# Kernel tuning notes

Hardware: AMD Instinct MI355X
Metric: run time of the kernel (lower is better)

Reference implementation:

```python
import jax, jax.numpy as jnp
import numpy as np

RES = 1024
NUM_ROOMS = 8
N_AGENTS = 5_000_000


def setup_inputs() -> dict:
    key = jax.random.key(0)
    k1, k2, k3 = jax.random.split(key, 3)
    agent_positions = jax.random.uniform(k1, (N_AGENTS, 2), dtype=jnp.float32)
    room_params = jax.random.uniform(k2, (NUM_ROOMS, 4), dtype=jnp.float32)
    # torch init: params[:, 2:] = params[:, 2:] * 0.1 + 0.05  (room sigmas)
    room_params = room_params.at[:, 2:].set(room_params[:, 2:] * 0.1 + 0.05)
    wall_density = jax.random.uniform(k3, (RES, RES), dtype=jnp.float32)
    return {
        "agent_positions": agent_positions,
        "room_params": room_params,
        "wall_density": wall_density,
    }


def reference(agent_positions, room_params, wall_density):
    res = wall_density.shape[0]
    lin = jnp.linspace(0.0, 1.0, res, dtype=wall_density.dtype)
    x_grid, y_grid = jnp.meshgrid(lin, lin, indexing="ij")  # [res,res]

    # Per-room Gaussian density maps, vectorized over rooms -> [R,res,res]
    cx = room_params[:, 0, None, None]
    cy = room_params[:, 1, None, None]
    sx = room_params[:, 2, None, None]
    sy = room_params[:, 3, None, None]
    spatial_layout = jnp.exp(
        -((x_grid - cx) ** 2 / (2.0 * sx**2) + (y_grid - cy) ** 2 / (2.0 * sy**2))
    )

    # Agent flow histogram via single fused scatter-add
    ix = jnp.clip((agent_positions[:, 0] * res).astype(jnp.int32), 0, res - 1)
    iy = jnp.clip((agent_positions[:, 1] * res).astype(jnp.int32), 0, res - 1)
    flow_field = jnp.zeros((res, res), dtype=wall_density.dtype).at[ix, iy].add(1.0)
    flow_field = flow_field / (flow_field.max() + 1e-6)

    dynamic_layout = spatial_layout * (1.0 - wall_density[None, :, :])
    return (dynamic_layout, flow_field)
```

## Files before the change

kernel.cpp:

```cpp
#include <hip/hip_runtime.h>

#define RES 1024
#define NROOMS 8
#define NBUCKETS 256
#define BINS_PER_BUCKET (4 * RES)
#define CAP 32768
#define SWPB 8
#define F4PT 8
#define AGB 8192

__global__ __launch_bounds__(512) void scatter_kernel(
    const float4* __restrict__ pos, int n4, int nagents,
    unsigned short* __restrict__ buf, unsigned int* __restrict__ cursor)
{
    __shared__ unsigned int   cnt[SWPB][NBUCKETS];
    __shared__ unsigned int   sbase[SWPB][NBUCKETS];
    __shared__ unsigned int   pstart[NBUCKETS];
    __shared__ unsigned int   ptotal[NBUCKETS];
    __shared__ unsigned int   gbase[NBUCKETS];
    __shared__ unsigned int   wsum[4];
    __shared__ unsigned short staged[AGB];

    int tid  = threadIdx.x;
    int wv   = tid >> 6;
    int lane = tid & 63;

    #pragma unroll
    for (int i = 0; i < (SWPB * NBUCKETS) / 512; ++i)
        ((unsigned int*)cnt)[tid + 512 * i] = 0u;
    __syncthreads();

    unsigned int   code[2 * F4PT];
    unsigned short rank[2 * F4PT];
    int base4 = blockIdx.x * (AGB / 2);
    #pragma unroll
    for (int k = 0; k < F4PT; ++k) {
        int i4 = base4 + (k << 9) + tid;
        if (i4 < n4) {
            float4 p = pos[i4];
            int ix0 = min(max((int)(p.x * 1024.0f), 0), 1023);
            int iy0 = min(max((int)(p.y * 1024.0f), 0), 1023);
            int ix1 = min(max((int)(p.z * 1024.0f), 0), 1023);
            int iy1 = min(max((int)(p.w * 1024.0f), 0), 1023);
            unsigned int b0 = (unsigned int)(ix0 >> 2);
            unsigned int b1 = (unsigned int)(ix1 >> 2);
            code[2 * k]     = (b0 << 16) | (unsigned int)(((ix0 & 3) << 10) | iy0);
            code[2 * k + 1] = (b1 << 16) | (unsigned int)(((ix1 & 3) << 10) | iy1);
            rank[2 * k]     = (unsigned short)atomicAdd(&cnt[wv][b0], 1u);
            rank[2 * k + 1] = (unsigned short)atomicAdd(&cnt[wv][b1], 1u);
        } else {
            code[2 * k] = 0xFFFFFFFFu;
            code[2 * k + 1] = 0xFFFFFFFFu;
        }
    }
    __syncthreads();

    unsigned int run = 0;
    if (tid < NBUCKETS) {
        #pragma unroll
        for (int w = 0; w < SWPB; ++w) {
            unsigned int c = cnt[w][tid];
            sbase[w][tid] = run;
            run += c;
        }
        ptotal[tid] = run;
        gbase[tid]  = run ? atomicAdd(&cursor[tid], run) : 0u;
        unsigned int t = run;
        #pragma unroll
        for (int off = 1; off < 64; off <<= 1) {
            unsigned int v = (unsigned int)__shfl_up((int)t, off, 64);
            if (lane >= off) t += v;
        }
        if (lane == 63) wsum[wv] = t;
        pstart[tid] = t - run;
    }
    __syncthreads();
    if (tid < NBUCKETS) {
        unsigned int off = 0;
        #pragma unroll
        for (int w = 0; w < 3; ++w) if (w < wv) off += wsum[w];
        unsigned int ps = pstart[tid] + off;
        pstart[tid] = ps;
        #pragma unroll
        for (int w = 0; w < SWPB; ++w) sbase[w][tid] += ps;
    }
    __syncthreads();

    #pragma unroll
    for (int k = 0; k < 2 * F4PT; ++k) {
        unsigned int cd = code[k];
        if (cd != 0xFFFFFFFFu) {
            unsigned int b = cd >> 16;
            staged[sbase[wv][b] + rank[k]] = (unsigned short)(cd & 0xFFFFu);
        }
    }
    __syncthreads();

    #pragma unroll 4
    for (int bb = 0; bb < 32; ++bb) {
        int b = (wv << 5) + bb;
        unsigned int n  = ptotal[b];
        unsigned int ps = pstart[b];
        unsigned int gb = gbase[b];
        for (unsigned int e = lane; e < n; e += 64) {
            unsigned int p = gb + e;
            if (p < CAP) buf[b * CAP + p] = staged[ps + e];
        }
    }

    if (blockIdx.x == 0 && tid == 0 && (nagents & 1)) {
        const float* t = (const float*)pos;
        float px = t[2 * (nagents - 1)];
        float py = t[2 * (nagents - 1) + 1];
        int ix = min(max((int)(px * 1024.0f), 0), 1023);
        int iy = min(max((int)(py * 1024.0f), 0), 1023);
        unsigned int b = (unsigned int)(ix >> 2);
        unsigned int p = atomicAdd(&cursor[b], 1u);
        if (p < CAP) buf[b * CAP + p] = (unsigned short)(((ix & 3) << 10) | iy);
    }
}

__global__ __launch_bounds__(1024) void hist_build_kernel(
    const unsigned short* __restrict__ buf,
    const unsigned int* __restrict__ cursor,
    unsigned int* __restrict__ counts,
    unsigned int* __restrict__ out_max)
{
    __shared__ __align__(16) unsigned int h[BINS_PER_BUCKET];
    int b = blockIdx.x, tid = threadIdx.x;
    #pragma unroll
    for (int i = 0; i < BINS_PER_BUCKET / 1024; ++i) h[tid + 1024 * i] = 0u;
    __syncthreads();

    unsigned int n = min(cursor[b], (unsigned int)CAP);
    const unsigned short* seg = buf + (size_t)b * CAP;
    unsigned int n2 = n & ~1u;
    for (unsigned int i = 2 * tid; i < n2; i += 2048) {
        unsigned int u = *(const unsigned int*)(seg + i);
        atomicAdd(&h[u & 0xFFFFu], 1u);
        atomicAdd(&h[u >> 16], 1u);
    }
    if (tid == 0 && (n & 1)) atomicAdd(&h[seg[n - 1]], 1u);
    __syncthreads();

    uint4 v = ((const uint4*)h)[tid];
    ((uint4*)counts)[(size_t)b * (BINS_PER_BUCKET / 4) + tid] = v;
    unsigned int m = max(max(v.x, v.y), max(v.z, v.w));
    #pragma unroll
    for (int off = 32; off > 0; off >>= 1)
        m = max(m, (unsigned int)__shfl_down((int)m, off, 64));
    __shared__ unsigned int sm[16];
    if ((tid & 63) == 0) sm[tid >> 6] = m;
    __syncthreads();
    if (tid == 0) {
        #pragma unroll
        for (int w = 1; w < 16; ++w) m = max(m, sm[w]);
        atomicMax(out_max, m);
    }
}

__global__ __launch_bounds__(256) void hist_atomic_kernel(
    const float4* __restrict__ pos, int n4, int nagents,
    unsigned int* __restrict__ counts)
{
    int idx = blockIdx.x * blockDim.x + threadIdx.x;
    int stride = gridDim.x * blockDim.x;
    for (int i = idx; i < n4; i += stride) {
        float4 p = pos[i];
        int ix0 = min(max((int)(p.x * 1024.0f), 0), 1023);
        int iy0 = min(max((int)(p.y * 1024.0f), 0), 1023);
        int ix1 = min(max((int)(p.z * 1024.0f), 0), 1023);
        int iy1 = min(max((int)(p.w * 1024.0f), 0), 1023);
        atomicAdd(&counts[(ix0 << 10) + iy0], 1u);
        atomicAdd(&counts[(ix1 << 10) + iy1], 1u);
    }
    if (idx == 0 && (nagents & 1)) {
        const float* t = (const float*)pos;
        int ix = min(max((int)(t[2 * (nagents - 1)] * 1024.0f), 0), 1023);
        int iy = min(max((int)(t[2 * (nagents - 1) + 1] * 1024.0f), 0), 1023);
        atomicAdd(&counts[(ix << 10) + iy], 1u);
    }
}

__global__ __launch_bounds__(256) void max_kernel(
    const uint4* __restrict__ counts, unsigned int* __restrict__ out_max)
{
    int idx = blockIdx.x * blockDim.x + threadIdx.x;
    int stride = gridDim.x * blockDim.x;
    unsigned int m = 0;
    const int n4 = (RES * RES) / 4;
    for (int i = idx; i < n4; i += stride) {
        uint4 c = counts[i];
        m = max(m, max(max(c.x, c.y), max(c.z, c.w)));
    }
    #pragma unroll
    for (int off = 32; off > 0; off >>= 1)
        m = max(m, (unsigned int)__shfl_down((int)m, off, 64));
    __shared__ unsigned int sm[4];
    if ((threadIdx.x & 63) == 0) sm[threadIdx.x >> 6] = m;
    __syncthreads();
    if (threadIdx.x == 0) {
        m = max(max(sm[0], sm[1]), max(sm[2], sm[3]));
        atomicMax(out_max, m);
    }
}

__global__ __launch_bounds__(256) void final_kernel(
    const float* __restrict__ room_params,
    const float4* __restrict__ wall,
    float4* __restrict__ dyn,
    float* __restrict__ flow,
    const unsigned int* __restrict__ maxp)
{
    int idx = blockIdx.x * blockDim.x + threadIdx.x;
    int i  = idx >> 8;
    int j0 = (idx & 255) << 2;

    const float inv1023 = 1.0f / 1023.0f;
    float x  = (float)i * inv1023;
    float y0 = (float)(j0 + 0) * inv1023;
    float y1 = (float)(j0 + 1) * inv1023;
    float y2 = (float)(j0 + 2) * inv1023;
    float y3 = (float)(j0 + 3) * inv1023;

    float4 w = wall[idx];
    float omx = 1.0f - w.x;
    float omy = 1.0f - w.y;
    float omz = 1.0f - w.z;
    float omw = 1.0f - w.w;

    uint4 c = ((const uint4*)flow)[idx];
    float inv = 1.0f / ((float)(*maxp) + 1e-6f);
    ((float4*)flow)[idx] = make_float4((float)c.x * inv, (float)c.y * inv,
                                       (float)c.z * inv, (float)c.w * inv);

    const int plane4 = (RES * RES) / 4;
    #pragma unroll
    for (int r = 0; r < NROOMS; ++r) {
        float cx = room_params[4 * r + 0];
        float cy = room_params[4 * r + 1];
        float sx = room_params[4 * r + 2];
        float sy = room_params[4 * r + 3];
        float isx = 1.0f / (2.0f * sx * sx);
        float isy = 1.0f / (2.0f * sy * sy);
        float dx = x - cx;
        float ax = dx * dx * isx;
        float d0 = y0 - cy, d1 = y1 - cy, d2 = y2 - cy, d3 = y3 - cy;
        float4 d;
        d.x = __expf(-(ax + d0 * d0 * isy)) * omx;
        d.y = __expf(-(ax + d1 * d1 * isy)) * omy;
        d.z = __expf(-(ax + d2 * d2 * isy)) * omz;
        d.w = __expf(-(ax + d3 * d3 * isy)) * omw;
        dyn[(size_t)r * plane4 + idx] = d;
    }
}

extern "C" void kernel_launch(void* const* d_in, const int* in_sizes, int n_in,
                              void* d_out, int out_size, void* d_ws, size_t ws_size,
                              hipStream_t stream) {
    const float* agents      = (const float*)d_in[0];
    const float* room_params = (const float*)d_in[1];
    const float* wall        = (const float*)d_in[2];

    float* dyn  = (float*)d_out;
    float* flow = (float*)d_out + (size_t)NROOMS * RES * RES;
    unsigned int* counts = (unsigned int*)flow;

    int nagents = in_sizes[0] / 2;
    int n4 = nagents / 2;

    size_t need = 2048 + (size_t)NBUCKETS * CAP * sizeof(unsigned short);

    if (ws_size >= need) {
        unsigned int*   cursor = (unsigned int*)d_ws;
        unsigned int*   maxp   = (unsigned int*)((char*)d_ws + 1024);
        unsigned short* buf    = (unsigned short*)((char*)d_ws + 2048);

        hipMemsetAsync(d_ws, 0, 2048, stream);
        int nblk = (n4 + (AGB / 2) - 1) / (AGB / 2);
        scatter_kernel<<<nblk, 512, 0, stream>>>((const float4*)agents, n4, nagents,
                                                 buf, cursor);
        hist_build_kernel<<<NBUCKETS, 1024, 0, stream>>>(buf, cursor, counts, maxp);
        final_kernel<<<(RES * RES / 4) / 256, 256, 0, stream>>>(
            room_params, (const float4*)wall, (float4*)dyn, flow, maxp);
    } else {
        unsigned int* maxp = (unsigned int*)d_ws;
        hipMemsetAsync(flow, 0, (size_t)RES * RES * sizeof(float), stream);
        hipMemsetAsync(maxp, 0, sizeof(unsigned int), stream);
        hist_atomic_kernel<<<1280, 256, 0, stream>>>((const float4*)agents, n4, nagents, counts);
        max_kernel<<<256, 256, 0, stream>>>((const uint4*)counts, maxp);
        final_kernel<<<(RES * RES / 4) / 256, 256, 0, stream>>>(
            room_params, (const float4*)wall, (float4*)dyn, flow, maxp);
    }
}
```

Baseline: 124.1 us.

## Fuse dynamic-layout computation into scatter kernel and shrink final pass to normalization

New measurement: 120.5 us. 2.9% less time.

```diff
diff --git a/kernel.cpp b/kernel.cpp
--- a/kernel.cpp
+++ b/kernel.cpp
@@ -6,12 +6,57 @@
 #define BINS_PER_BUCKET (4 * RES)
 #define CAP 32768
 #define SWPB 8
-#define F4PT 8
 #define AGB 8192
+
+typedef unsigned int u32x4 __attribute__((ext_vector_type(4)));
+
+__device__ __forceinline__ void dyn_cell(
+    const float* __restrict__ room_params,
+    const float4* __restrict__ wall,
+    float4* __restrict__ dyn, int idx)
+{
+    int i  = idx >> 8;
+    int j0 = (idx & 255) << 2;
+    const float inv1023 = 1.0f / 1023.0f;
+    float x  = (float)i * inv1023;
+    float y0 = (float)(j0 + 0) * inv1023;
+    float y1 = (float)(j0 + 1) * inv1023;
+    float y2 = (float)(j0 + 2) * inv1023;
+    float y3 = (float)(j0 + 3) * inv1023;
+
+    float4 w = wall[idx];
+    float omx = 1.0f - w.x;
+    float omy = 1.0f - w.y;
+    float omz = 1.0f - w.z;
+    float omw = 1.0f - w.w;
+
+    const int plane4 = (RES * RES) / 4;
+    #pragma unroll
+    for (int r = 0; r < NROOMS; ++r) {
+        float cx = room_params[4 * r + 0];
+        float cy = room_params[4 * r + 1];
+        float sx = room_params[4 * r + 2];
+        float sy = room_params[4 * r + 3];
+        float isx = 1.0f / (2.0f * sx * sx);
+        float isy = 1.0f / (2.0f * sy * sy);
+        float dx = x - cx;
+        float ax = dx * dx * isx;
+        float d0 = y0 - cy, d1 = y1 - cy, d2 = y2 - cy, d3 = y3 - cy;
+        float4 d;
+        d.x = __expf(-(ax + d0 * d0 * isy)) * omx;
+        d.y = __expf(-(ax + d1 * d1 * isy)) * omy;
+        d.z = __expf(-(ax + d2 * d2 * isy)) * omz;
+        d.w = __expf(-(ax + d3 * d3 * isy)) * omw;
+        dyn[(size_t)r * plane4 + idx] = d;
+    }
+}
 
 __global__ __launch_bounds__(512) void scatter_kernel(
     const float4* __restrict__ pos, int n4, int nagents,
-    unsigned short* __restrict__ buf, unsigned int* __restrict__ cursor)
+    unsigned short* __restrict__ buf, unsigned int* __restrict__ cursor,
+    const float* __restrict__ room_params,
+    const float4* __restrict__ wall,
+    float4* __restrict__ dyn)
 {
     __shared__ unsigned int   cnt[SWPB][NBUCKETS];
     __shared__ unsigned int   sbase[SWPB][NBUCKETS];
@@ -30,11 +75,11 @@
         ((unsigned int*)cnt)[tid + 512 * i] = 0u;
     __syncthreads();
 
-    unsigned int   code[2 * F4PT];
-    unsigned short rank[2 * F4PT];
+    unsigned int   code[16];
+    unsigned short rank[16];
     int base4 = blockIdx.x * (AGB / 2);
     #pragma unroll
-    for (int k = 0; k < F4PT; ++k) {
+    for (int k = 0; k < 8; ++k) {
         int i4 = base4 + (k << 9) + tid;
         if (i4 < n4) {
             float4 p = pos[i4];
@@ -55,8 +100,8 @@
     }
     __syncthreads();
 
-    unsigned int run = 0;
     if (tid < NBUCKETS) {
+        unsigned int run = 0;
         #pragma unroll
         for (int w = 0; w < SWPB; ++w) {
             unsigned int c = cnt[w][tid];
@@ -87,7 +132,7 @@
     __syncthreads();
 
     #pragma unroll
-    for (int k = 0; k < 2 * F4PT; ++k) {
+    for (int k = 0; k < 16; ++k) {
         unsigned int cd = code[k];
         if (cd != 0xFFFFFFFFu) {
             unsigned int b = cd >> 16;
@@ -108,6 +153,10 @@
         }
     }
 
+    int gid = blockIdx.x * 512 + tid;
+    if (gid < (RES * RES) / 4)
+        dyn_cell(room_params, wall, dyn, gid);
+
     if (blockIdx.x == 0 && tid == 0 && (nagents & 1)) {
         const float* t = (const float*)pos;
         float px = t[2 * (nagents - 1)];
@@ -143,8 +192,8 @@
     if (tid == 0 && (n & 1)) atomicAdd(&h[seg[n - 1]], 1u);
     __syncthreads();
 
-    uint4 v = ((const uint4*)h)[tid];
-    ((uint4*)counts)[(size_t)b * (BINS_PER_BUCKET / 4) + tid] = v;
+    u32x4 v = ((const u32x4*)h)[tid];
+    ((u32x4*)counts)[(size_t)b * (BINS_PER_BUCKET / 4) + tid] = v;
     unsigned int m = max(max(v.x, v.y), max(v.z, v.w));
     #pragma unroll
     for (int off = 32; off > 0; off >>= 1)
@@ -157,6 +206,16 @@
         for (int w = 1; w < 16; ++w) m = max(m, sm[w]);
         atomicMax(out_max, m);
     }
+}
+
+__global__ __launch_bounds__(256) void norm_kernel(
+    float* __restrict__ flow, const unsigned int* __restrict__ maxp)
+{
+    int idx = blockIdx.x * blockDim.x + threadIdx.x;
+    uint4 c = ((const uint4*)flow)[idx];
+    float inv = 1.0f / ((float)(*maxp) + 1e-6f);
+    ((float4*)flow)[idx] = make_float4((float)c.x * inv, (float)c.y * inv,
+                                       (float)c.z * inv, (float)c.w * inv);
 }
 
 __global__ __launch_bounds__(256) void hist_atomic_kernel(
@@ -205,7 +264,7 @@
     }
 }
 
-__global__ __launch_bounds__(256) void final_kernel(
+__global__ __launch_bounds__(256) void final_full_kernel(
     const float* __restrict__ room_params,
     const float4* __restrict__ wall,
     float4* __restrict__ dyn,
@@ -213,46 +272,11 @@
     const unsigned int* __restrict__ maxp)
 {
     int idx = blockIdx.x * blockDim.x + threadIdx.x;
-    int i  = idx >> 8;
-    int j0 = (idx & 255) << 2;
-
-    const float inv1023 = 1.0f / 1023.0f;
-    float x  = (float)i * inv1023;
-    float y0 = (float)(j0 + 0) * inv1023;
-    float y1 = (float)(j0 + 1) * inv1023;
-    float y2 = (float)(j0 + 2) * inv1023;
-    float y3 = (float)(j0 + 3) * inv1023;
-
-    float4 w = wall[idx];
-    float omx = 1.0f - w.x;
-    float omy = 1.0f - w.y;
-    float omz = 1.0f - w.z;
-    float omw = 1.0f - w.w;
-
     uint4 c = ((const uint4*)flow)[idx];
     float inv = 1.0f / ((float)(*maxp) + 1e-6f);
     ((float4*)flow)[idx] = make_float4((float)c.x * inv, (float)c.y * inv,
                                        (float)c.z * inv, (float)c.w * inv);
-
-    const int plane4 = (RES * RES) / 4;
-    #pragma unroll
-    for (int r = 0; r < NROOMS; ++r) {
-        float cx = room_params[4 * r + 0];
-        float cy = room_params[4 * r + 1];
-        float sx = room_params[4 * r + 2];
-        float sy = room_params[4 * r + 3];
-        float isx = 1.0f / (2.0f * sx * sx);
-        float isy = 1.0f / (2.0f * sy * sy);
-        float dx = x - cx;
-        float ax = dx * dx * isx;
-        float d0 = y0 - cy, d1 = y1 - cy, d2 = y2 - cy, d3 = y3 - cy;
-        float4 d;
-        d.x = __expf(-(ax + d0 * d0 * isy)) * omx;
-        d.y = __expf(-(ax + d1 * d1 * isy)) * omy;
-        d.z = __expf(-(ax + d2 * d2 * isy)) * omz;
-        d.w = __expf(-(ax + d3 * d3 * isy)) * omw;
-        dyn[(size_t)r * plane4 + idx] = d;
-    }
+    dyn_cell(room_params, wall, dyn, idx);
 }
 
 extern "C" void kernel_launch(void* const* d_in, const int* in_sizes, int n_in,
@@ -276,20 +300,20 @@
         unsigned int*   maxp   = (unsigned int*)((char*)d_ws + 1024);
         unsigned short* buf    = (unsigned short*)((char*)d_ws + 2048);
 
-        hipMemsetAsync(d_ws, 0, 2048, stream);
+        (void)hipMemsetAsync(d_ws, 0, 2048, stream);
         int nblk = (n4 + (AGB / 2) - 1) / (AGB / 2);
-        scatter_kernel<<<nblk, 512, 0, stream>>>((const float4*)agents, n4, nagents,
-                                                 buf, cursor);
+        scatter_kernel<<<nblk, 512, 0, stream>>>(
+            (const float4*)agents, n4, nagents, buf, cursor,
+            room_params, (const float4*)wall, (float4*)dyn);
         hist_build_kernel<<<NBUCKETS, 1024, 0, stream>>>(buf, cursor, counts, maxp);
-        final_kernel<<<(RES * RES / 4) / 256, 256, 0, stream>>>(
-            room_params, (const float4*)wall, (float4*)dyn, flow, maxp);
+        norm_kernel<<<(RES * RES / 4) / 256, 256, 0, stream>>>(flow, maxp);
     } else {
         unsigned int* maxp = (unsigned int*)d_ws;
-        hipMemsetAsync(flow, 0, (size_t)RES * RES * sizeof(float), stream);
-        hipMemsetAsync(maxp, 0, sizeof(unsigned int), stream);
+        (void)hipMemsetAsync(flow, 0, (size_t)RES * RES * sizeof(float), stream);
+        (void)hipMemsetAsync(maxp, 0, sizeof(unsigned int), stream);
         hist_atomic_kernel<<<1280, 256, 0, stream>>>((const float4*)agents, n4, nagents, counts);
         max_kernel<<<256, 256, 0, stream>>>((const uint4*)counts, maxp);
-        final_kernel<<<(RES * RES / 4) / 256, 256, 0, stream>>>(
+        final_full_kernel<<<(RES * RES / 4) / 256, 256, 0, stream>>>(
             room_params, (const float4*)wall, (float4*)dyn, flow, maxp);
     }
 }
```
